# Performance work log

Measured on AMD Instinct MI355X. Metric: run time of the kernel, lower is better.

The kernel has to match this reference:

```python
import jax, jax.numpy as jnp
import numpy as np
import math
from jax import lax

HID, H, K = 1024, 8, 4
D = HID // H
B, T = 2, 2048
CLAMP_MAX = 0.999995
LN_EPS = 1e-5

def _logit(x):
    x = min(max(x, 1e-06), 1 - 1e-06)
    return math.log(x / (1 - x))

def setup_inputs() -> dict:
    key = jax.random.key(0)
    ks = jax.random.split(key, 8)
    def xavier(k, fan_in, fan_out):
        s = math.sqrt(2.0 / (fan_in + fan_out))
        return jax.random.normal(k, (fan_in, fan_out), jnp.float32) * s
    x = jax.random.normal(ks[0], (B, T, HID), jnp.float32)
    mask = jnp.ones((B, T), jnp.float32)
    Wq = xavier(ks[1], HID, HID)
    Wk = xavier(ks[2], HID, HID)
    Wv = xavier(ks[3], HID, HID)
    Wb = xavier(ks[4], HID, H)
    bb = jnp.full((H,), _logit(0.99), jnp.float32)
    Wm = xavier(ks[5], HID, H * K)
    bm = jnp.zeros((H * K,), jnp.float32)
    Wo = xavier(ks[6], HID, HID)
    bo = jnp.zeros((HID,), jnp.float32)
    base = np.array([_logit(math.exp(-1.0 / t)) for t in [16.0, 64.0, 256.0, 1024.0]], np.float32)
    base_logit = jnp.asarray(np.tile(base[None, :], (H, 1)))  # (H, K)
    ln_g = jnp.ones((HID,), jnp.float32)
    ln_b = jnp.zeros((HID,), jnp.float32)
    return dict(x=x, mask=mask, Wq=Wq, Wk=Wk, Wv=Wv, Wb=Wb, bb=bb, Wm=Wm, bm=bm,
                Wo=Wo, bo=bo, base_logit=base_logit, ln_g=ln_g, ln_b=ln_b)

def _delta_scan(q, k, v, beta, mix, mask, base_logit):
    # q,k,v: (B,T,H,D); beta: (B,T,H); mix: (B,T,H,K); mask: (B,T)
    b, t = q.shape[0], q.shape[1]
    base_r = jax.nn.sigmoid(base_logit)  # (H,K)
    state0 = jnp.zeros((b, H, K, D, D), jnp.float32)

    def step(state, inp):
        q_t, k_t, v_t, b_t, mix_t, m_t = inp
        valid = (m_t > 0)[:, None, None, None, None]            # (B,1,1,1,1)
        r_eff = jnp.clip(b_t[:, :, None] * base_r[None], 0.0, CLAMP_MAX)  # (B,H,K)
        outer = jnp.einsum('bhd,bhe->bhde', k_t, v_t)[:, :, None]          # (B,H,1,D,D)
        new_state = jnp.where(valid, state * r_eff[..., None, None] + outer, state)
        o_scales = jnp.einsum('bhd,bhkde->bhke', q_t, new_state)           # (B,H,K,D)
        w = jax.nn.softmax(mix_t, axis=-1)                                  # (B,H,K)
        o_t = jnp.sum(w[..., None] * o_scales, axis=2)                      # (B,H,D)
        o_t = o_t * (m_t > 0)[:, None, None].astype(o_t.dtype)
        return new_state, o_t

    xs = (jnp.moveaxis(q, 1, 0), jnp.moveaxis(k, 1, 0), jnp.moveaxis(v, 1, 0),
          jnp.moveaxis(beta, 1, 0), jnp.moveaxis(mix, 1, 0), jnp.moveaxis(mask, 1, 0))
    _, outs = lax.scan(step, state0, xs)       # (T,B,H,D)
    return jnp.moveaxis(outs, 0, 1)            # (B,T,H,D)

def reference(x, mask, Wq, Wk, Wv, Wb, bb, Wm, bm, Wo, bo, base_logit, ln_g, ln_b):
    b, t, _ = x.shape
    def elu1(z):
        return jax.nn.elu(z) + 1.0
    q = elu1((x @ Wq).reshape(b, t, H, D))
    k = elu1((x @ Wk).reshape(b, t, H, D))
    v = (x @ Wv).reshape(b, t, H, D)
    beta = jax.nn.sigmoid(x @ Wb + bb)               # (B,T,H)
    mix = (x @ Wm + bm).reshape(b, t, H, K)          # (B,T,H,K)
    head_out = _delta_scan(q, k, v, beta, mix, mask, base_logit)  # (B,T,H,D)
    out = head_out.reshape(b, t, HID) @ Wo + bo
    y = x + out                                       # residual (dropout in eval mode)
    mu = jnp.mean(y, axis=-1, keepdims=True)
    var = jnp.mean((y - mu) ** 2, axis=-1, keepdims=True)
    return (y - mu) * lax.rsqrt(var + LN_EPS) * ln_g + ln_b
```

## Files before the change

### kernel.cpp

```cpp
#include <hip/hip_runtime.h>
#include <hip/hip_bf16.h>
#include <math.h>

#define TSEQ 2048
#define NHID 1024

typedef float f32x4 __attribute__((ext_vector_type(4)));
typedef __bf16 bf16x8 __attribute__((ext_vector_type(8)));

static __device__ __forceinline__ unsigned short f2bf(float f) {
  unsigned u = __float_as_uint(f);
  u += 0x7fffu + ((u >> 16) & 1u);
  return (unsigned short)(u >> 16);
}
static __device__ __forceinline__ float bf2f(unsigned short h) {
  return __uint_as_float(((unsigned)h) << 16);
}

#define GLDS16(g, l) __builtin_amdgcn_global_load_lds( \
    (const __attribute__((address_space(1))) unsigned int*)(g), \
    (__attribute__((address_space(3))) unsigned int*)(l), 16, 0, 0)

__global__ __launch_bounds__(256) void transpose_all_kernel(
    const float* __restrict__ Wq, const float* __restrict__ Wk,
    const float* __restrict__ Wv, const float* __restrict__ Wo,
    const float* __restrict__ Wb, const float* __restrict__ Wm,
    unsigned short* __restrict__ Wqkvt, unsigned short* __restrict__ Wto,
    float* __restrict__ Wtf) {
  int m = blockIdx.z;
  int tx = threadIdx.x, ty = threadIdx.y;
  if (m == 4) {
    int blk = blockIdx.y * 32 + blockIdx.x;
    if (blk >= 160) return;
    int id = blk * 256 + ty * 32 + tx;
    int o = id >> 10, i = id & 1023;
    Wtf[id] = (o < 8) ? Wb[i * 8 + o] : Wm[i * 32 + (o - 8)];
    return;
  }
  __shared__ float tile[32][33];
  const float* W;
  unsigned short* Wt;
  if (m == 0)      { W = Wq; Wt = Wqkvt; }
  else if (m == 1) { W = Wk; Wt = Wqkvt + 1024 * 1024; }
  else if (m == 2) { W = Wv; Wt = Wqkvt + 2 * 1024 * 1024; }
  else             { W = Wo; Wt = Wto; }
  int bx = blockIdx.x * 32;
  int by = blockIdx.y * 32;
#pragma unroll
  for (int i = 0; i < 32; i += 8)
    tile[ty + i][tx] = W[(size_t)(by + ty + i) * NHID + bx + tx];
  __syncthreads();
#pragma unroll
  for (int i = 0; i < 32; i += 8)
    Wt[(size_t)(bx + ty + i) * NHID + by + tx] = f2bf(tile[tx][ty + i]);
}

template <int MODE>
__global__ __launch_bounds__(256) void gemm_pipe_kernel(
    const unsigned short* __restrict__ A, const unsigned short* __restrict__ Bt,
    unsigned short* __restrict__ Oq, unsigned short* __restrict__ Ok,
    unsigned short* __restrict__ Ov, float* __restrict__ Pbase) {
  __shared__ __align__(16) unsigned short As[3 * 4096];
  __shared__ __align__(16) unsigned short Bs[3 * 4096];
  const int tid = threadIdx.x;
  const int lane = tid & 63;
  const int wave = tid >> 6;
  const int wr = wave >> 1, wc = wave & 1;
  const int rowBase = blockIdx.y * 128;
  const int colBase = blockIdx.x * 128;
  const int NT = (MODE == 0) ? 32 : 16;
  const int kOff = (MODE == 0) ? 0 : blockIdx.z * 512;

  const int c0 = wave * 128 + lane;
  const int c1 = c0 + 64;
  const int r0 = c0 >> 2, kc0 = (c0 & 3) ^ ((r0 >> 1) & 3);
  const int r1 = c1 >> 2, kc1 = (c1 & 3) ^ ((r1 >> 1) & 3);
  const unsigned short* gA0 = A + (size_t)(rowBase + r0) * 1024 + kOff + kc0 * 8;
  const unsigned short* gA1 = A + (size_t)(rowBase + r1) * 1024 + kOff + kc1 * 8;
  const unsigned short* gB0 = Bt + (size_t)(colBase + r0) * 1024 + kOff + kc0 * 8;
  const unsigned short* gB1 = Bt + (size_t)(colBase + r1) * 1024 + kOff + kc1 * 8;
  const int wofs = wave * 1024;

  const int kq = lane >> 4;
  const int r16 = lane & 15;

  f32x4 acc[4][4] = {};

#define STAGE(buf, k0)                                       \
  do {                                                       \
    GLDS16(gA0 + (k0), &As[(buf) * 4096 + wofs]);            \
    GLDS16(gA1 + (k0), &As[(buf) * 4096 + wofs + 512]);      \
    GLDS16(gB0 + (k0), &Bs[(buf) * 4096 + wofs]);            \
    GLDS16(gB1 + (k0), &Bs[(buf) * 4096 + wofs + 512]);      \
  } while (0)

  STAGE(0, 0);
  STAGE(1, 32);
  int cur = 0, stg = 2;
  for (int t = 0; t < NT; ++t) {
    if (t < NT - 2) {
      STAGE(stg, (t + 2) * 32);
      asm volatile("s_waitcnt vmcnt(8)" ::: "memory");
    } else if (t == NT - 2) {
      asm volatile("s_waitcnt vmcnt(4)" ::: "memory");
    } else {
      asm volatile("s_waitcnt vmcnt(0)" ::: "memory");
    }
    __builtin_amdgcn_s_barrier();
    asm volatile("" ::: "memory");
    const unsigned short* Ac = &As[cur * 4096];
    const unsigned short* Bc = &Bs[cur * 4096];
    bf16x8 af[4], bfr[4];
#pragma unroll
    for (int m = 0; m < 4; ++m) {
      int row = wr * 64 + m * 16 + r16;
      af[m] = *(const bf16x8*)(Ac + row * 32 + (kq ^ ((row >> 1) & 3)) * 8);
      int colr = wc * 64 + m * 16 + r16;
      bfr[m] = *(const bf16x8*)(Bc + colr * 32 + (kq ^ ((colr >> 1) & 3)) * 8);
    }
#pragma unroll
    for (int m = 0; m < 4; ++m)
#pragma unroll
      for (int n = 0; n < 4; ++n)
        acc[m][n] = __builtin_amdgcn_mfma_f32_16x16x32_bf16(af[m], bfr[n], acc[m][n], 0, 0, 0);
    asm volatile("" ::: "memory");
    __builtin_amdgcn_s_barrier();
    asm volatile("" ::: "memory");
    cur = (cur == 2) ? 0 : cur + 1;
    stg = (stg == 2) ? 0 : stg + 1;
  }
#undef STAGE

  const int r4 = (lane >> 4) * 4;
  if (MODE == 1) {
    float* P = Pbase + (size_t)blockIdx.z * 4096 * 1024;
#pragma unroll
    for (int m = 0; m < 4; ++m)
#pragma unroll
      for (int n = 0; n < 4; ++n) {
        int col = colBase + wc * 64 + n * 16 + r16;
#pragma unroll
        for (int j = 0; j < 4; ++j) {
          int row = rowBase + wr * 64 + m * 16 + r4 + j;
          P[(size_t)row * 1024 + col] = acc[m][n][j];
        }
      }
  } else {
    unsigned short* outp;
    int cb;
    bool elu;
    if (colBase < 1024)      { outp = Oq; cb = colBase;        elu = true;  }
    else if (colBase < 2048) { outp = Ok; cb = colBase - 1024; elu = true;  }
    else                     { outp = Ov; cb = colBase - 2048; elu = false; }
#pragma unroll
    for (int m = 0; m < 4; ++m)
#pragma unroll
      for (int n = 0; n < 4; ++n) {
        int col = cb + wc * 64 + n * 16 + r16;
#pragma unroll
        for (int j = 0; j < 4; ++j) {
          int row = rowBase + wr * 64 + m * 16 + r4 + j;
          float v = acc[m][n][j];
          if (elu) v = (v > 0.f) ? (v + 1.f) : expf(v);
          outp[(size_t)row * 1024 + col] = f2bf(v);
        }
      }
  }
}

__global__ __launch_bounds__(256) void rw8_kernel(const float* __restrict__ x,
    const float* __restrict__ Wt, const float* __restrict__ bb,
    const float* __restrict__ bm, const float* __restrict__ base_logit,
    float* __restrict__ R, float* __restrict__ Wsm,
    unsigned short* __restrict__ Xb) {
  __shared__ float xs[8][1024];
  __shared__ float outs[8][40];
  int row0 = blockIdx.x * 8;
  int tid = threadIdx.x;
#pragma unroll
  for (int r = 0; r < 8; ++r) {
    float4 xv = *(const float4*)(x + (size_t)(row0 + r) * 1024 + tid * 4);
    *(float4*)(&xs[r][tid * 4]) = xv;
    ushort4 xo;
    xo.x = f2bf(xv.x); xo.y = f2bf(xv.y); xo.z = f2bf(xv.z); xo.w = f2bf(xv.w);
    *(ushort4*)(Xb + (size_t)(row0 + r) * 1024 + tid * 4) = xo;
  }
  __syncthreads();
  int wave = tid >> 6, lane = tid & 63;
  for (int o = wave; o < 40; o += 4) {
    const float* wr = Wt + o * 1024;
    float w[16];
#pragma unroll
    for (int it = 0; it < 16; ++it) w[it] = wr[it * 64 + lane];
#pragma unroll
    for (int r = 0; r < 8; ++r) {
      float sum = 0.f;
#pragma unroll
      for (int it = 0; it < 16; ++it) sum += xs[r][it * 64 + lane] * w[it];
#pragma unroll
      for (int off = 32; off > 0; off >>= 1) sum += __shfl_down(sum, off);
      if (lane == 0) outs[r][o] = sum;
    }
  }
  __syncthreads();
  {
    int r = tid >> 5, j = tid & 31;
    int row = row0 + r;
    int h = j >> 2;
    float beta = 1.f / (1.f + expf(-(outs[r][h] + bb[h])));
    float br = 1.f / (1.f + expf(-base_logit[j]));
    float rr = fminf(fmaxf(beta * br, 0.f), 0.999995f);
    float mval = outs[r][8 + j] + bm[j];
    float mx = fmaxf(mval, __shfl_xor(mval, 1));
    mx = fmaxf(mx, __shfl_xor(mx, 2));
    float ex = expf(mval - mx);
    float ssum = ex + __shfl_xor(ex, 1);
    ssum += __shfl_xor(ssum, 2);
    R[(size_t)row * 32 + j] = rr;
    Wsm[(size_t)row * 32 + j] = ex / ssum;
  }
}

__global__ __launch_bounds__(256) void decay2_kernel(const float* __restrict__ R,
    const float* __restrict__ Wsm, const float* __restrict__ mask,
    float* __restrict__ WA, float* __restrict__ IA, float* __restrict__ DU,
    float* __restrict__ AC) {
  int wave = threadIdx.x >> 6, lane = threadIdx.x & 63;
  int id = blockIdx.x * 4 + wave;
  int c = id & 15, k = (id >> 4) & 3, bh = id >> 6;
  int b = bh >> 3, h = bh & 7;
  int row0 = b * TSEQ + c * 128 + 2 * lane;
  float m0 = mask[row0], m1 = mask[row0 + 1];
  size_t i0 = (size_t)row0 * 32 + h * 4 + k;
  float rr0 = (m0 > 0.f) ? R[i0] : 1.f;
  float rr1 = (m1 > 0.f) ? R[i0 + 32] : 1.f;
  float incl = rr0 * rr1;
#pragma unroll
  for (int off = 1; off < 64; off <<= 1) {
    float o = __shfl_up(incl, off);
    if (lane >= off) incl *= o;
  }
  float excl = __shfl_up(incl, 1);
  if (lane == 0) excl = 1.f;
  float a0 = fmaxf(excl * rr0, 1e-25f);
  float a1 = fmaxf(a0 * rr1, 1e-25f);
  float aC = __shfl(a1, 63);
  if (lane == 63) AC[(bh * 16 + c) * 4 + k] = a1;
  bool v0 = m0 > 0.f, v1 = m1 > 0.f;
  float w0 = Wsm[i0], w1 = Wsm[i0 + 32];
  int dub = ((bh * 16 + c) * 4 + k) * 128 + 2 * lane;
  WA[i0] = v0 ? w0 * a0 : 0.f;
  WA[i0 + 32] = v1 ? w1 * a1 : 0.f;
  IA[i0] = v0 ? 1.f / a0 : 0.f;
  IA[i0 + 32] = v1 ? 1.f / a1 : 0.f;
  DU[dub] = v0 ? aC / a0 : 0.f;
  DU[dub + 1] = v1 ? aC / a1 : 0.f;
}

#define KV_SLOT(j, d) (((j) ^ ((d) & 7) ^ (((d) >> 3) & 7)) << 4)

__global__ __launch_bounds__(512) void chunkA_kernel(
    const unsigned short* __restrict__ Qb, const unsigned short* __restrict__ Kb,
    const unsigned short* __restrict__ Vb,
    const float* __restrict__ WA, const float* __restrict__ IA,
    const float* __restrict__ DU,
    unsigned short* __restrict__ Olb, unsigned short* __restrict__ UT) {
  __shared__ __align__(16) char KTl[32768];
  __shared__ __align__(16) char VTl[32768];
  __shared__ __align__(16) char Pl[32768];
  __shared__ __align__(16) float WAl[128][4];
  __shared__ __align__(16) float IAl[128][4];
  __shared__ float DUl[4][128];

  int wg = blockIdx.x;
  int bh = wg >> 4, c = wg & 15;
  int b = bh >> 3, h = bh & 7;
  int t0 = c * 128;
  int tid = threadIdx.x;
  int lane = tid & 63, wave = tid >> 6;
  int wbase = wave * 16;
  int l15 = lane & 15, lq = lane >> 4;

  const size_t qkvbase = ((size_t)b * TSEQ + t0) * 1024 + h * 128;

  for (int it = 0; it < 2; ++it) {
    int ci = tid + it * 512;
    int t = (ci >> 4) * 2, s = ci & 15;
    bf16x8 k0 = *(const bf16x8*)(Kb + qkvbase + (size_t)t * 1024 + s * 8);
    bf16x8 k1 = *(const bf16x8*)(Kb + qkvbase + (size_t)(t + 1) * 1024 + s * 8);
    bf16x8 v0 = *(const bf16x8*)(Vb + qkvbase + (size_t)t * 1024 + s * 8);
    bf16x8 v1 = *(const bf16x8*)(Vb + qkvbase + (size_t)(t + 1) * 1024 + s * 8);
    const unsigned short* k0u = (const unsigned short*)&k0;
    const unsigned short* k1u = (const unsigned short*)&k1;
    const unsigned short* v0u = (const unsigned short*)&v0;
    const unsigned short* v1u = (const unsigned short*)&v1;
#pragma unroll
    for (int e = 0; e < 8; ++e) {
      int d = s * 8 + e;
      int off = d * 256 + (((t >> 3) ^ (d & 7) ^ ((d >> 3) & 7)) << 4) + (t & 7) * 2;
      *(unsigned int*)(KTl + off) = (unsigned)k0u[e] | ((unsigned)k1u[e] << 16);
      *(unsigned int*)(VTl + off) = (unsigned)v0u[e] | ((unsigned)v1u[e] << 16);
    }
  }
  {
    int t = tid >> 2, k = tid & 3;
    size_t idx = ((size_t)b * TSEQ + t0 + t) * 32 + h * 4 + k;
    WAl[t][k] = WA[idx];
    IAl[t][k] = IA[idx];
    int k2 = tid >> 7, j = tid & 127;
    DUl[k2][j] = DU[((bh * 16 + c) * 4 + k2) * 128 + j];
  }
  __syncthreads();

  bf16x8 qf[4];
#pragma unroll
  for (int ds = 0; ds < 4; ++ds)
    qf[ds] = *(const bf16x8*)(Qb + qkvbase + (size_t)(wbase + l15) * 1024 + ds * 32 + lq * 8);
  f32x4 accP[8];
#pragma unroll
  for (int jf = 0; jf < 8; ++jf) {
    f32x4 a = {};
#pragma unroll
    for (int ds = 0; ds < 4; ++ds) {
      bf16x8 kfrag = *(const bf16x8*)(Kb + qkvbase + (size_t)(jf * 16 + l15) * 1024 + ds * 32 + lq * 8);
      a = __builtin_amdgcn_mfma_f32_16x16x32_bf16(qf[ds], kfrag, a, 0, 0, 0);
    }
    accP[jf] = a;
  }

  float4 wa4[4];
#pragma unroll
  for (int jj = 0; jj < 4; ++jj)
    wa4[jj] = *(const float4*)&WAl[wbase + lq * 4 + jj][0];
#pragma unroll
  for (int jf = 0; jf < 8; ++jf) {
    float4 ia4 = *(const float4*)&IAl[jf * 16 + l15][0];
#pragma unroll
    for (int jj = 0; jj < 4; ++jj) {
      int tl = wbase + lq * 4 + jj;
      int jl = jf * 16 + l15;
      float m = 0.f;
      if (jl <= tl)
        m = wa4[jj].x * ia4.x + wa4[jj].y * ia4.y + wa4[jj].z * ia4.z + wa4[jj].w * ia4.w;
      float pv = accP[jf][jj] * m;
      int off = tl * 256 + (((jl >> 3) ^ (tl & 7)) << 4) + (jl & 7) * 2;
      *(unsigned short*)(Pl + off) = f2bf(pv);
    }
  }

  bf16x8 pf[4];
#pragma unroll
  for (int js = 0; js < 4; ++js) {
    int tl = wbase + l15;
    int slot = js * 4 + lq;
    pf[js] = *(const bf16x8*)(Pl + tl * 256 + ((slot ^ (tl & 7)) << 4));
  }
#pragma unroll
  for (int dvf = 0; dvf < 8; ++dvf) {
    f32x4 a = {};
    int dv = dvf * 16 + l15;
#pragma unroll
    for (int js = 0; js < 4; ++js) {
      int slot = js * 4 + lq;
      bf16x8 vfrag = *(const bf16x8*)(VTl + dv * 256 + KV_SLOT(slot, dv));
      a = __builtin_amdgcn_mfma_f32_16x16x32_bf16(pf[js], vfrag, a, 0, 0, 0);
    }
#pragma unroll
    for (int jj = 0; jj < 4; ++jj) {
      int tl = wbase + lq * 4 + jj;
      Olb[((size_t)b * TSEQ + t0 + tl) * 1024 + h * 128 + dv] = f2bf(a[jj]);
    }
  }

  if (c < 15) {
#pragma unroll 1
    for (int k = 0; k < 4; ++k) {
      f32x4 accU[8] = {};
#pragma unroll 1
      for (int js = 0; js < 4; ++js) {
        int dvr = wbase + l15;
        int slot = js * 4 + lq;
        bf16x8 af = *(const bf16x8*)(VTl + dvr * 256 + KV_SLOT(slot, dvr));
        int j0 = js * 32 + lq * 8;
        bf16x8 afs;
#pragma unroll
        for (int e = 0; e < 8; ++e)
          afs[e] = (__bf16)((float)af[e] * DUl[k][j0 + e]);
#pragma unroll
        for (int dkf = 0; dkf < 8; ++dkf) {
          int dk = dkf * 16 + l15;
          bf16x8 kf = *(const bf16x8*)(KTl + dk * 256 + KV_SLOT(slot, dk));
          accU[dkf] = __builtin_amdgcn_mfma_f32_16x16x32_bf16(afs, kf, accU[dkf], 0, 0, 0);
        }
      }
      size_t ub = (((size_t)bh * 16 + c) * 4 + k) * 16384;
#pragma unroll
      for (int dkf = 0; dkf < 8; ++dkf) {
        int dk = dkf * 16 + l15;
#pragma unroll
        for (int jj = 0; jj < 4; ++jj) {
          int dvr = wbase + lq * 4 + jj;
          UT[ub + (size_t)dvr * 128 + dk] = f2bf(accU[dkf][jj]);
        }
      }
    }
  }
}

__global__ __launch_bounds__(256) void chainB_kernel(const unsigned short* __restrict__ UT,
    const float* __restrict__ AC, unsigned short* __restrict__ S0T) {
  int id = blockIdx.x * 256 + threadIdx.x;
  int dk = id & 127;
  int dv = (id >> 7) & 127;
  int k = (id >> 14) & 3;
  int bh = id >> 16;
  size_t elem = (size_t)dv * 128 + dk;
  float S = 0.f;
#pragma unroll 1
  for (int c = 0; c < 15; ++c) {
    size_t ub = (((size_t)bh * 16 + c) * 4 + k) * 16384;
    float u = bf2f(UT[ub + elem]);
    float aC = AC[(bh * 16 + c) * 4 + k];
    S = aC * S + u;
    size_t sb = (((size_t)bh * 16 + (c + 1)) * 4 + k) * 16384;
    S0T[sb + elem] = f2bf(S);
  }
}

__global__ __launch_bounds__(512) void chunkC_kernel(const unsigned short* __restrict__ Qb,
    const unsigned short* __restrict__ S0T, const float* __restrict__ WA,
    const unsigned short* __restrict__ Olb, unsigned short* __restrict__ Ob) {
  __shared__ __align__(16) char Sl[32768];
  int wg = blockIdx.x;
  int bh = wg >> 4, c = wg & 15;
  int b = bh >> 3, h = bh & 7;
  int t0 = c * 128;
  int tid = threadIdx.x, lane = tid & 63, wave = tid >> 6;
  int l15 = lane & 15, lq = lane >> 4, wbase = wave * 16;
  size_t qbase = ((size_t)b * TSEQ + t0) * 1024 + h * 128;

  f32x4 accO[8] = {};
  if (c > 0) {
    int tl = wbase + l15;
#pragma unroll 1
    for (int k = 0; k < 4; ++k) {
      __syncthreads();
      size_t sb = (((size_t)bh * 16 + c) * 4 + k) * 16384;
      for (int it = 0; it < 4; ++it) {
        int ci = tid + it * 512;
        int dv = ci >> 4, s = ci & 15;
        bf16x8 vv = *(const bf16x8*)(S0T + sb + (size_t)dv * 128 + s * 8);
        *(bf16x8*)(Sl + dv * 256 + ((s ^ (dv & 7)) << 4)) = vv;
      }
      __syncthreads();
      float sc = WA[((size_t)b * TSEQ + t0 + tl) * 32 + h * 4 + k];
#pragma unroll 1
      for (int ds = 0; ds < 4; ++ds) {
        bf16x8 qf = *(const bf16x8*)(Qb + qbase + (size_t)tl * 1024 + ds * 32 + lq * 8);
        bf16x8 qs;
#pragma unroll
        for (int e = 0; e < 8; ++e) qs[e] = (__bf16)((float)qf[e] * sc);
#pragma unroll
        for (int dvf = 0; dvf < 8; ++dvf) {
          int dv = dvf * 16 + l15;
          int slot = ds * 4 + lq;
          bf16x8 sf = *(const bf16x8*)(Sl + dv * 256 + ((slot ^ (dv & 7)) << 4));
          accO[dvf] = __builtin_amdgcn_mfma_f32_16x16x32_bf16(qs, sf, accO[dvf], 0, 0, 0);
        }
      }
    }
  }
#pragma unroll
  for (int dvf = 0; dvf < 8; ++dvf) {
    int dv = dvf * 16 + l15;
#pragma unroll
    for (int jj = 0; jj < 4; ++jj) {
      int tl = wbase + lq * 4 + jj;
      size_t off = ((size_t)b * TSEQ + t0 + tl) * 1024 + h * 128 + dv;
      Ob[off] = f2bf(accO[dvf][jj] + bf2f(Olb[off]));
    }
  }
}

__global__ __launch_bounds__(256) void ln_kernel(const float* __restrict__ Pbase,
    const float* __restrict__ bo, const float* __restrict__ xres,
    const float* __restrict__ g, const float* __restrict__ bta,
    float* __restrict__ out) {
  int row = blockIdx.x;
  int tid = threadIdx.x;
  int lane = tid & 63, wave = tid >> 6;
  __shared__ float red[8];
  size_t base = (size_t)row * 1024 + tid * 4;
  const size_t PS = (size_t)4096 * 1024;
  float4 a = *(const float4*)(Pbase + base);
  float4 b2 = *(const float4*)(Pbase + PS + base);
  float4 xv = *(const float4*)(xres + base);
  float4 bv = *(const float4*)(bo + tid * 4);
  float4 v;
  v.x = a.x + b2.x + bv.x + xv.x;
  v.y = a.y + b2.y + bv.y + xv.y;
  v.z = a.z + b2.z + bv.z + xv.z;
  v.w = a.w + b2.w + bv.w + xv.w;
  float sum = v.x + v.y + v.z + v.w;
#pragma unroll
  for (int off = 32; off > 0; off >>= 1) sum += __shfl_down(sum, off);
  if (lane == 0) red[wave] = sum;
  __syncthreads();
  float mu = (red[0] + red[1] + red[2] + red[3]) * (1.f / 1024.f);
  float4 d;
  d.x = v.x - mu; d.y = v.y - mu; d.z = v.z - mu; d.w = v.w - mu;
  float sq = d.x * d.x + d.y * d.y + d.z * d.z + d.w * d.w;
#pragma unroll
  for (int off = 32; off > 0; off >>= 1) sq += __shfl_down(sq, off);
  __syncthreads();
  if (lane == 0) red[4 + wave] = sq;
  __syncthreads();
  float var = (red[4] + red[5] + red[6] + red[7]) * (1.f / 1024.f);
  float inv = rsqrtf(var + 1e-5f);
  float4 gg = *(const float4*)(g + tid * 4);
  float4 bb4 = *(const float4*)(bta + tid * 4);
  float4 o;
  o.x = d.x * inv * gg.x + bb4.x;
  o.y = d.y * inv * gg.y + bb4.y;
  o.z = d.z * inv * gg.z + bb4.z;
  o.w = d.w * inv * gg.w + bb4.w;
  *(float4*)(out + (size_t)row * 1024 + tid * 4) = o;
}

extern "C" void kernel_launch(void* const* d_in, const int* in_sizes, int n_in,
                              void* d_out, int out_size, void* d_ws, size_t ws_size,
                              hipStream_t stream) {
  const float* x    = (const float*)d_in[0];
  const float* mask = (const float*)d_in[1];
  const float* Wq   = (const float*)d_in[2];
  const float* Wk   = (const float*)d_in[3];
  const float* Wv   = (const float*)d_in[4];
  const float* Wb   = (const float*)d_in[5];
  const float* bb   = (const float*)d_in[6];
  const float* Wm   = (const float*)d_in[7];
  const float* bm   = (const float*)d_in[8];
  const float* Wo   = (const float*)d_in[9];
  const float* bo   = (const float*)d_in[10];
  const float* base_logit = (const float*)d_in[11];
  const float* ln_g = (const float*)d_in[12];
  const float* ln_b = (const float*)d_in[13];

  char* ws = (char*)d_ws;
  const size_t MB = 1024u * 1024u;
  unsigned short* Xb    = (unsigned short*)(ws + 0);
  unsigned short* Wqkvt = (unsigned short*)(ws + 8 * MB);
  unsigned short* Wto   = (unsigned short*)(ws + 14 * MB);
  float* Rf  = (float*)(ws + 16 * MB);
  float* Wsf = (float*)(ws + 16 * MB + 512 * 1024);
  float* WAf = (float*)(ws + 17 * MB);
  float* IAf = (float*)(ws + 17 * MB + 512 * 1024);
  float* DUf = (float*)(ws + 18 * MB);
  float* ACf = (float*)(ws + 18 * MB + 512 * 1024);
  float* Wtf = (float*)(ws + 18 * MB + 768 * 1024);
  unsigned short* Qb  = (unsigned short*)(ws + 19 * MB);
  unsigned short* Kb  = (unsigned short*)(ws + 27 * MB);
  unsigned short* Vb  = (unsigned short*)(ws + 35 * MB);
  unsigned short* Olb = (unsigned short*)(ws + 43 * MB);
  unsigned short* Ob  = (unsigned short*)(ws + 51 * MB);
  unsigned short* UTb = (unsigned short*)(ws + 59 * MB);
  unsigned short* S0T = (unsigned short*)(ws + 91 * MB);
  float* Pp = (float*)(ws + 59 * MB);
  if (ws_size < 131 * MB) return;

  dim3 tb(32, 8), tg(32, 32, 5);
  transpose_all_kernel<<<tg, tb, 0, stream>>>(Wq, Wk, Wv, Wo, Wb, Wm, Wqkvt, Wto, Wtf);

  rw8_kernel<<<512, 256, 0, stream>>>(x, Wtf, bb, bm, base_logit, Rf, Wsf, Xb);
  decay2_kernel<<<256, 256, 0, stream>>>(Rf, Wsf, mask, WAf, IAf, DUf, ACf);

  dim3 gqkv(24, 32);
  gemm_pipe_kernel<0><<<gqkv, 256, 0, stream>>>(Xb, Wqkvt, Qb, Kb, Vb, nullptr);

  chunkA_kernel<<<256, 512, 0, stream>>>(Qb, Kb, Vb, WAf, IAf, DUf, Olb, UTb);
  chainB_kernel<<<4096, 256, 0, stream>>>(UTb, ACf, S0T);
  chunkC_kernel<<<256, 512, 0, stream>>>(Qb, S0T, WAf, Olb, Ob);

  dim3 gwo(8, 32, 2);
  gemm_pipe_kernel<1><<<gwo, 256, 0, stream>>>(Ob, Wto, nullptr, nullptr, nullptr, Pp);

  ln_kernel<<<4096, 256, 0, stream>>>(Pp, bo, x, ln_g, ln_b, (float*)d_out);
}
```

Baseline: 168.9 us.

## Store split-K partials in bf16, vectorize chain scan, use direct LDS loads

The split-K output-projection partials are now written and read as bf16 instead of fp32, which halves the traffic between the Wo GEMM and the layernorm kernel. The chunk-state chain kernel now processes four elements per thread with vector loads and stores, so it launches a quarter as many blocks. chunkC stages the state tiles into LDS with global_load_lds instead of going through registers, and precomputes the swizzled offsets once. The price is extra bf16 rounding on the partials before the residual add and layernorm, which lowers output precision.

Measured after the change: 163.0 us. -3.5%, faster.

```diff
diff --git a/kernel.cpp b/kernel.cpp
--- a/kernel.cpp
+++ b/kernel.cpp
@@ -59,7 +59,7 @@
 __global__ __launch_bounds__(256) void gemm_pipe_kernel(
     const unsigned short* __restrict__ A, const unsigned short* __restrict__ Bt,
     unsigned short* __restrict__ Oq, unsigned short* __restrict__ Ok,
-    unsigned short* __restrict__ Ov, float* __restrict__ Pbase) {
+    unsigned short* __restrict__ Ov, unsigned short* __restrict__ Pbase) {
   __shared__ __align__(16) unsigned short As[3 * 4096];
   __shared__ __align__(16) unsigned short Bs[3 * 4096];
   const int tid = threadIdx.x;
@@ -133,7 +133,7 @@
 
   const int r4 = (lane >> 4) * 4;
   if (MODE == 1) {
-    float* P = Pbase + (size_t)blockIdx.z * 4096 * 1024;
+    unsigned short* P = Pbase + (size_t)blockIdx.z * 4096 * 1024;
 #pragma unroll
     for (int m = 0; m < 4; ++m)
 #pragma unroll
@@ -142,7 +142,7 @@
 #pragma unroll
         for (int j = 0; j < 4; ++j) {
           int row = rowBase + wr * 64 + m * 16 + r4 + j;
-          P[(size_t)row * 1024 + col] = acc[m][n][j];
+          P[(size_t)row * 1024 + col] = f2bf(acc[m][n][j]);
         }
       }
   } else {
@@ -410,20 +410,25 @@
 __global__ __launch_bounds__(256) void chainB_kernel(const unsigned short* __restrict__ UT,
     const float* __restrict__ AC, unsigned short* __restrict__ S0T) {
   int id = blockIdx.x * 256 + threadIdx.x;
-  int dk = id & 127;
-  int dv = (id >> 7) & 127;
-  int k = (id >> 14) & 3;
-  int bh = id >> 16;
-  size_t elem = (size_t)dv * 128 + dk;
-  float S = 0.f;
+  int dk4 = id & 31;
+  int dv = (id >> 5) & 127;
+  int k = (id >> 12) & 3;
+  int bh = id >> 14;
+  size_t elem = (size_t)dv * 128 + dk4 * 4;
+  float S0 = 0.f, S1 = 0.f, S2 = 0.f, S3 = 0.f;
 #pragma unroll 1
   for (int c = 0; c < 15; ++c) {
-    size_t ub = (((size_t)bh * 16 + c) * 4 + k) * 16384;
-    float u = bf2f(UT[ub + elem]);
+    size_t ub = (((size_t)bh * 16 + c) * 4 + k) * 16384 + elem;
+    ushort4 u = *(const ushort4*)(UT + ub);
     float aC = AC[(bh * 16 + c) * 4 + k];
-    S = aC * S + u;
-    size_t sb = (((size_t)bh * 16 + (c + 1)) * 4 + k) * 16384;
-    S0T[sb + elem] = f2bf(S);
+    S0 = aC * S0 + bf2f(u.x);
+    S1 = aC * S1 + bf2f(u.y);
+    S2 = aC * S2 + bf2f(u.z);
+    S3 = aC * S3 + bf2f(u.w);
+    size_t sb = (((size_t)bh * 16 + (c + 1)) * 4 + k) * 16384 + elem;
+    ushort4 o;
+    o.x = f2bf(S0); o.y = f2bf(S1); o.z = f2bf(S2); o.w = f2bf(S3);
+    *(ushort4*)(S0T + sb) = o;
   }
 }
 
@@ -442,16 +447,22 @@
   f32x4 accO[8] = {};
   if (c > 0) {
     int tl = wbase + l15;
+    size_t so[4];
+#pragma unroll
+    for (int it = 0; it < 4; ++it) {
+      int ci = tid + it * 512;
+      int dv = ci >> 4, s = ci & 15;
+      so[it] = (size_t)dv * 128 + (size_t)(s ^ (dv & 7)) * 8;
+    }
 #pragma unroll 1
     for (int k = 0; k < 4; ++k) {
       __syncthreads();
       size_t sb = (((size_t)bh * 16 + c) * 4 + k) * 16384;
-      for (int it = 0; it < 4; ++it) {
-        int ci = tid + it * 512;
-        int dv = ci >> 4, s = ci & 15;
-        bf16x8 vv = *(const bf16x8*)(S0T + sb + (size_t)dv * 128 + s * 8);
-        *(bf16x8*)(Sl + dv * 256 + ((s ^ (dv & 7)) << 4)) = vv;
-      }
+      GLDS16(S0T + sb + so[0], (unsigned short*)(Sl + wave * 1024));
+      GLDS16(S0T + sb + so[1], (unsigned short*)(Sl + 8192 + wave * 1024));
+      GLDS16(S0T + sb + so[2], (unsigned short*)(Sl + 16384 + wave * 1024));
+      GLDS16(S0T + sb + so[3], (unsigned short*)(Sl + 24576 + wave * 1024));
+      asm volatile("s_waitcnt vmcnt(0)" ::: "memory");
       __syncthreads();
       float sc = WA[((size_t)b * TSEQ + t0 + tl) * 32 + h * 4 + k];
 #pragma unroll 1
@@ -482,7 +493,7 @@
   }
 }
 
-__global__ __launch_bounds__(256) void ln_kernel(const float* __restrict__ Pbase,
+__global__ __launch_bounds__(256) void ln_kernel(const unsigned short* __restrict__ Pbase,
     const float* __restrict__ bo, const float* __restrict__ xres,
     const float* __restrict__ g, const float* __restrict__ bta,
     float* __restrict__ out) {
@@ -492,15 +503,15 @@
   __shared__ float red[8];
   size_t base = (size_t)row * 1024 + tid * 4;
   const size_t PS = (size_t)4096 * 1024;
-  float4 a = *(const float4*)(Pbase + base);
-  float4 b2 = *(const float4*)(Pbase + PS + base);
+  ushort4 a = *(const ushort4*)(Pbase + base);
+  ushort4 b2 = *(const ushort4*)(Pbase + PS + base);
   float4 xv = *(const float4*)(xres + base);
   float4 bv = *(const float4*)(bo + tid * 4);
   float4 v;
-  v.x = a.x + b2.x + bv.x + xv.x;
-  v.y = a.y + b2.y + bv.y + xv.y;
-  v.z = a.z + b2.z + bv.z + xv.z;
-  v.w = a.w + b2.w + bv.w + xv.w;
+  v.x = bf2f(a.x) + bf2f(b2.x) + bv.x + xv.x;
+  v.y = bf2f(a.y) + bf2f(b2.y) + bv.y + xv.y;
+  v.z = bf2f(a.z) + bf2f(b2.z) + bv.z + xv.z;
+  v.w = bf2f(a.w) + bf2f(b2.w) + bv.w + xv.w;
   float sum = v.x + v.y + v.z + v.w;
 #pragma unroll
   for (int off = 32; off > 0; off >>= 1) sum += __shfl_down(sum, off);
@@ -564,7 +575,7 @@
   unsigned short* Ob  = (unsigned short*)(ws + 51 * MB);
   unsigned short* UTb = (unsigned short*)(ws + 59 * MB);
   unsigned short* S0T = (unsigned short*)(ws + 91 * MB);
-  float* Pp = (float*)(ws + 59 * MB);
+  unsigned short* Pp = (unsigned short*)(ws + 59 * MB);
   if (ws_size < 131 * MB) return;
 
   dim3 tb(32, 8), tg(32, 32, 5);
@@ -577,7 +588,7 @@
   gemm_pipe_kernel<0><<<gqkv, 256, 0, stream>>>(Xb, Wqkvt, Qb, Kb, Vb, nullptr);
 
   chunkA_kernel<<<256, 512, 0, stream>>>(Qb, Kb, Vb, WAf, IAf, DUf, Olb, UTb);
-  chainB_kernel<<<4096, 256, 0, stream>>>(UTb, ACf, S0T);
+  chainB_kernel<<<1024, 256, 0, stream>>>(UTb, ACf, S0T);
   chunkC_kernel<<<256, 512, 0, stream>>>(Qb, S0T, WAf, Olb, Ob);
 
   dim3 gwo(8, 32, 2);
```
